# Kernel tuning notes

Hardware: AMD Instinct MI355X
Metric: run time of the kernel (lower is better)

The kernel has to match this reference:

```python
import jax, jax.numpy as jnp
import numpy as np

B, S, FEAT, H, DK, MAX_ITEMS = 8, 1024, 512, 8, 64, 200
LN_EPS = 1e-5
NEG = -999999999.0


def _build_mask(seq_len):
    # rows before T = S-(maxItems+1) cannot see the tail block [T:];
    # tail rows T..S-2 cannot see columns >= their own index (strict upper wedge).
    T = seq_len - (MAX_ITEMS + 1)
    i = jnp.arange(seq_len)[:, None]
    j = jnp.arange(seq_len)[None, :]
    blocked = ((i < T) & (j >= T)) | ((i >= T) & (i <= seq_len - 2) & (j >= i))
    return jnp.where(blocked, NEG, 0.0).astype(jnp.float32)  # [S, S]


def setup_inputs() -> dict:
    key = jax.random.key(0)
    ks = jax.random.split(key, 6)
    def init(k, shape, fan_in):
        return (jax.random.normal(k, shape, jnp.float32) / np.sqrt(fan_in)).astype(jnp.float32)
    return {
        "x": jax.random.normal(ks[0], (B, S, FEAT), jnp.float32),
        "ln_gamma": jnp.ones((FEAT,), jnp.float32),
        "ln_beta": jnp.zeros((FEAT,), jnp.float32),
        "WQ": init(ks[1], (H, FEAT, DK), FEAT), "bq": jnp.zeros((H, DK), jnp.float32),
        "WK": init(ks[2], (H, FEAT, DK), FEAT), "bk": jnp.zeros((H, DK), jnp.float32),
        "WV": init(ks[3], (H, FEAT, DK), FEAT), "bv": jnp.zeros((H, DK), jnp.float32),
        "WO": init(ks[4], (H * DK, FEAT), H * DK), "bO": jnp.zeros((FEAT,), jnp.float32),
    }


def reference(x, ln_gamma, ln_beta, WQ, bq, WK, bk, WV, bv, WO, bO):
    b, s, f = x.shape
    # Pre-LN
    mu = jnp.mean(x, axis=-1, keepdims=True)
    var = jnp.mean((x - mu) ** 2, axis=-1, keepdims=True)
    xn = (x - mu) / jnp.sqrt(var + LN_EPS) * ln_gamma + ln_beta
    # per-head projections, heads stacked: [B, H, S, DK]
    q = jnp.einsum('bsf,hfd->bhsd', xn, WQ) + bq[None, :, None, :]
    k = jnp.einsum('bsf,hfd->bhsd', xn, WK) + bk[None, :, None, :]
    v = jnp.einsum('bsf,hfd->bhsd', xn, WV) + bv[None, :, None, :]
    scores = jnp.einsum('bhsd,bhtd->bhst', q, k) / np.sqrt(DK).astype(np.float32)
    scores = scores + _build_mask(s)[None, None, :, :]
    attn = jax.nn.softmax(scores, axis=-1)
    z = jnp.einsum('bhst,bhtd->bhsd', attn, v)           # [B, H, S, DK]
    z = jnp.transpose(z, (0, 2, 1, 3)).reshape(b, s, -1)  # concat heads -> [B, S, H*DK]
    return z @ WO + bO
```

## Files before the change

### kernel.cpp

```cpp
#include <hip/hip_runtime.h>

#define S_LEN 1024
#define FEATN 512
#define NH    8
#define DKN   64
#define T_CUT 823
#define LDP   76

typedef __attribute__((ext_vector_type(8))) short v8s;
typedef __attribute__((ext_vector_type(4))) float v4f;
typedef unsigned short u16;

__device__ __forceinline__ float bf2f(u16 u) {
    unsigned v = ((unsigned)u) << 16; float f; __builtin_memcpy(&f, &v, 4); return f;
}
__device__ __forceinline__ u16 f2bf(float f) {
    unsigned v; __builtin_memcpy(&v, &f, 4);
    v += 0x7fffu + ((v >> 16) & 1u);
    return (u16)(v >> 16);
}
__device__ __forceinline__ v4f mfma16(v8s a, v8s b, v4f c) {
    return __builtin_amdgcn_mfma_f32_16x16x32_bf16(a, b, c, 0, 0, 0);
}
__device__ __forceinline__ unsigned cvt_pk_bf16(float a, float b) {
    unsigned r;
    asm("v_cvt_pk_bf16_f32 %0, %1, %2" : "=v"(r) : "v"(a), "v"(b));
    return r;
}

__device__ __forceinline__ int sniff_f32(const void* x) {
    const u16* xs = (const u16*)x;
    int wild = 0;
    #pragma unroll
    for (int i = 0; i < 64; i++) {
        float v = bf2f(xs[i]);
        float a = fabsf(v);
        wild |= (!(a <= 256.f)) | ((v != 0.f) & (a <= 1e-9f));
    }
    return wild;
}

__device__ __forceinline__ float read_in(const void* p, long idx, int fl) {
    return fl ? ((const float*)p)[idx] : bf2f(((const u16*)p)[idx]);
}

__global__ __launch_bounds__(256) void prep_kernel(
    const void* __restrict__ x, const void* __restrict__ lg,
    const void* __restrict__ lb,
    const void* __restrict__ WQ, const void* __restrict__ WK,
    const void* __restrict__ WV, const void* __restrict__ WO,
    u16* __restrict__ xn, u16* __restrict__ BtQKV, u16* __restrict__ BtO)
{
    __shared__ u16 ld[64 * 68];
    const int fl = sniff_f32(x);
    const int b = blockIdx.x, t = threadIdx.x;
    if (b < 192) {
        const int which = b >> 6, rem = b & 63, h = rem >> 3, ktile = rem & 7;
        const void* W = which == 0 ? WQ : (which == 1 ? WK : WV);
        const float sc = (which == 0) ? 0.125f : 1.f;
        #pragma unroll
        for (int i = 0; i < 16; i++) {
            int idx = i * 256 + t, r = idx >> 6, c = idx & 63;
            float v = read_in(W, (long)h * 512 * 64 + (long)(ktile * 64 + r) * 64 + c, fl);
            ld[c * 68 + r] = f2bf(v * sc);
        }
        __syncthreads();
        #pragma unroll
        for (int i = 0; i < 16; i++) {
            int idx = i * 256 + t, d = idx >> 6, kk = idx & 63;
            BtQKV[(long)(which * 512 + h * 64 + d) * 512 + ktile * 64 + kk] = ld[d * 68 + kk];
        }
    } else if (b < 256) {
        const int b2 = b - 192, ntile = b2 >> 3, ktile = b2 & 7;
        #pragma unroll
        for (int i = 0; i < 16; i++) {
            int idx = i * 256 + t, r = idx >> 6, c = idx & 63;
            float v = read_in(WO, (long)(ktile * 64 + r) * 512 + ntile * 64 + c, fl);
            ld[c * 68 + r] = f2bf(v);
        }
        __syncthreads();
        #pragma unroll
        for (int i = 0; i < 16; i++) {
            int idx = i * 256 + t, d = idx >> 6, kk = idx & 63;
            BtO[(long)(ntile * 64 + d) * 512 + ktile * 64 + kk] = ld[d * 68 + kk];
        }
    } else {
        const int w = t >> 6, l = t & 63;
        const int row = (b - 256) * 4 + w;
        float f[8];
        if (fl) {
            const float4* x4 = (const float4*)((const float*)x + (size_t)row * FEATN);
            float4 p0 = x4[l * 2], p1 = x4[l * 2 + 1];
            f[0] = p0.x; f[1] = p0.y; f[2] = p0.z; f[3] = p0.w;
            f[4] = p1.x; f[5] = p1.y; f[6] = p1.z; f[7] = p1.w;
        } else {
            const u16* xu = (const u16*)x + (size_t)row * FEATN + l * 8;
            #pragma unroll
            for (int j = 0; j < 8; j++) f[j] = bf2f(xu[j]);
        }
        float s = 0.f, sq = 0.f;
        #pragma unroll
        for (int j = 0; j < 8; j++) { s += f[j]; sq += f[j] * f[j]; }
        #pragma unroll
        for (int sh = 1; sh < 64; sh <<= 1) { s += __shfl_xor(s, sh); sq += __shfl_xor(sq, sh); }
        const float mu = s * (1.f / 512.f);
        const float var = sq * (1.f / 512.f) - mu * mu;
        const float rstd = rsqrtf(var + 1e-5f);
        u16 o8[8];
        #pragma unroll
        for (int j = 0; j < 8; j++) {
            float gg = read_in(lg, l * 8 + j, fl), bb = read_in(lb, l * 8 + j, fl);
            o8[j] = f2bf((f[j] - mu) * rstd * gg + bb);
        }
        *(v8s*)&xn[(size_t)row * FEATN + l * 8] = *(v8s*)o8;
    }
}

__global__ __launch_bounds__(256) void gemm128(
    const void* __restrict__ x,
    const u16* __restrict__ A, const u16* __restrict__ Bt,
    int N, int K, int mode,
    const void* __restrict__ bq, const void* __restrict__ bk,
    const void* __restrict__ bv,
    u16* __restrict__ qp, u16* __restrict__ kw, u16* __restrict__ vt,
    const void* __restrict__ bO, void* __restrict__ out)
{
    __shared__ __attribute__((aligned(16))) u16 lA[2][128 * 32];
    __shared__ __attribute__((aligned(16))) u16 lB[2][128 * 32];
    const int fl = sniff_f32(x);
    const int bid = blockIdx.x;
    const int xcd = bid & 7, sidx = bid >> 3;
    const int m0 = ((sidx & 7) + xcd * 8) * 128;
    const int n0 = (sidx >> 3) * 128;
    const int t = threadIdx.x;
    const int w = t >> 6, l = t & 63, quad = l >> 4, lr = l & 15;
    const int wr = w >> 1, wc = w & 1;
    v4f acc[4][4] = {};
    const int grow = w * 32 + (l >> 2);
    const int gcol = (l & 3) * 8;
    const u16* Ab = A  + (long)m0 * K;
    const u16* Bb = Bt + (long)n0 * K;

    auto stage = [&](int q, int k0) {
        #pragma unroll
        for (int i = 0; i < 2; i++) {
            __builtin_amdgcn_global_load_lds(
                (const __attribute__((address_space(1))) void*)
                    (Ab + (long)(grow + i * 16) * K + k0 + gcol),
                (__attribute__((address_space(3))) void*)&lA[q][(w * 32 + i * 16) * 32],
                16, 0, 0);
            __builtin_amdgcn_global_load_lds(
                (const __attribute__((address_space(1))) void*)
                    (Bb + (long)(grow + i * 16) * K + k0 + gcol),
                (__attribute__((address_space(3))) void*)&lB[q][(w * 32 + i * 16) * 32],
                16, 0, 0);
        }
    };
    stage(0, 0);
    __syncthreads();
    int cur = 0;
    for (int k0 = 0; k0 < K; k0 += 32) {
        if (k0 + 32 < K) stage(cur ^ 1, k0 + 32);
        v8s af[4], bf[4];
        #pragma unroll
        for (int i = 0; i < 4; i++) {
            af[i] = *(v8s*)&lA[cur][(wr * 64 + i * 16 + lr) * 32 + quad * 8];
            bf[i] = *(v8s*)&lB[cur][(wc * 64 + i * 16 + lr) * 32 + quad * 8];
        }
        #pragma unroll
        for (int i = 0; i < 4; i++)
            #pragma unroll
            for (int j = 0; j < 4; j++)
                acc[i][j] = mfma16(af[i], bf[j], acc[i][j]);
        __syncthreads();
        cur ^= 1;
    }
    #pragma unroll
    for (int i = 0; i < 4; i++)
    #pragma unroll
    for (int j = 0; j < 4; j++) {
        const int mbase = m0 + wr * 64 + i * 16 + quad * 4;
        const int n = n0 + wc * 64 + j * 16 + lr;
        if (mode == 0) {
            const int which = n >> 9, nn = n & 511, h = nn >> 6, d = nn & 63;
            const void* bias = which == 0 ? bq : (which == 1 ? bk : bv);
            const float bs = read_in(bias, nn, fl) * ((which == 0) ? 0.125f : 1.f);
            const int b = mbase >> 10, s = mbase & 1023;
            if (which != 1) {
                u16 v4_[4];
                #pragma unroll
                for (int r = 0; r < 4; r++) v4_[r] = f2bf(acc[i][j][r] + bs);
                u16* dstT = (which == 0) ? qp : vt;
                *(uint2*)&dstT[((size_t)((b * NH + h) * DKN + d)) * S_LEN + s] =
                    *(const uint2*)v4_;
            } else {
                #pragma unroll
                for (int r = 0; r < 4; r++)
                    kw[(((long)(b * NH + h)) * S_LEN + (s + r)) * DKN + d] =
                        f2bf(acc[i][j][r] + bs);
            }
        } else {
            const float bb = read_in(bO, n, fl);
            #pragma unroll
            for (int r = 0; r < 4; r++) {
                float ov = acc[i][j][r] + bb;
                if (fl) ((float*)out)[(long)(mbase + r) * N + n] = ov;
                else    ((u16*)out)[(long)(mbase + r) * N + n] = f2bf(ov);
            }
        }
    }
}

__global__ __launch_bounds__(256) void attn_kernel(
    const u16* __restrict__ qp, const u16* __restrict__ kw,
    const u16* __restrict__ vt, u16* __restrict__ zw)
{
    __shared__ __attribute__((aligned(16))) u16 lk[64 * LDP];
    __shared__ __attribute__((aligned(16))) u16 lv[64 * LDP];
    __shared__ __attribute__((aligned(16))) u16 lp[4][16 * LDP];
    const int bid = blockIdx.x;
    const int bh = bid & 63, qt = bid >> 6;
    const int q0 = qt * 64, qmax = q0 + 63;
    const int t = threadIdx.x, w = t >> 6, l = t & 63, quad = l >> 4, lr = l & 15;
    const int srow = t >> 2, scg = t & 3;
    const u16* Qp = qp + (size_t)bh * S_LEN * DKN;
    const u16* Kg = kw + (size_t)bh * S_LEN * DKN;
    const u16* Vt = vt + (size_t)bh * S_LEN * DKN;
    v8s aq[2];
    #pragma unroll
    for (int kf = 0; kf < 2; kf++) {
        u16 tmp[8];
        #pragma unroll
        for (int j = 0; j < 8; j++)
            tmp[j] = Qp[(size_t)(kf * 32 + quad * 8 + j) * S_LEN + q0 + w * 16 + lr];
        __builtin_memcpy(&aq[kf], tmp, 16);
    }
    v4f o[4] = {};
    v4f o1 = {};
    v8s vone;
    #pragma unroll
    for (int j = 0; j < 8; j++) vone[j] = (short)0x3f80;
    const int iq = q0 + w * 16 + quad * 4;
    const int i_row = q0 + w * 16 + lr;
    const int jlim = (i_row < T_CUT) ? T_CUT
                   : ((i_row <= S_LEN - 2) ? i_row : 0x40000000);
    const int mx_ = (T_CUT > qmax) ? T_CUT : qmax;
    const int ntiles = (qmax > S_LEN - 2) ? 16 : ((mx_ + 63) >> 6);
    v8s kr0 = *(const v8s*)&Kg[srow * DKN + scg * 8];
    v8s kr1 = *(const v8s*)&Kg[srow * DKN + 32 + scg * 8];
    v8s vr0 = *(const v8s*)&Vt[srow * S_LEN + scg * 8];
    v8s vr1 = *(const v8s*)&Vt[srow * S_LEN + 32 + scg * 8];

    for (int it = 0; it < ntiles; ++it) {
        const int kt0 = it * 64;
        __syncthreads();
        *(v8s*)&lk[srow * LDP + scg * 8]      = kr0;
        *(v8s*)&lk[srow * LDP + 32 + scg * 8] = kr1;
        *(v8s*)&lv[srow * LDP + scg * 8]      = vr0;
        *(v8s*)&lv[srow * LDP + 32 + scg * 8] = vr1;
        __syncthreads();
        if (it + 1 < ntiles) {
            kr0 = *(const v8s*)&Kg[(kt0 + 64 + srow) * DKN + scg * 8];
            kr1 = *(const v8s*)&Kg[(kt0 + 64 + srow) * DKN + 32 + scg * 8];
            vr0 = *(const v8s*)&Vt[srow * S_LEN + kt0 + 64 + scg * 8];
            vr1 = *(const v8s*)&Vt[srow * S_LEN + kt0 + 96 + scg * 8];
        }
        v4f sf[4];
        __builtin_amdgcn_s_setprio(1);
        #pragma unroll
        for (int cb = 0; cb < 4; cb++) {
            v8s b0 = *(v8s*)&lk[(cb * 16 + lr) * LDP + quad * 8];
            v8s b1 = *(v8s*)&lk[(cb * 16 + lr) * LDP + 32 + quad * 8];
            v4f z = {};
            z = mfma16(b0, aq[0], z);
            z = mfma16(b1, aq[1], z);
            sf[cb] = z;
        }
        __builtin_amdgcn_s_setprio(0);
        u16* lpw = lp[w];
        const int kt63 = kt0 + 63;
        const bool tmask = ((q0 < T_CUT) && (kt63 >= T_CUT)) ||
                           ((qmax >= T_CUT) && (kt63 >= q0));
        const int jbase = jlim - kt0 - quad * 4;
        #pragma unroll
        for (int cb = 0; cb < 4; cb++) {
            float e[4];
            #pragma unroll
            for (int r = 0; r < 4; r++) {
                float ev = __expf(sf[cb][r]);
                if (tmask) ev = (cb * 16 + r >= jbase) ? 0.f : ev;
                e[r] = ev;
            }
            uint2 pk;
            pk.x = cvt_pk_bf16(e[0], e[1]);
            pk.y = cvt_pk_bf16(e[2], e[3]);
            *(uint2*)&lpw[lr * LDP + cb * 16 + quad * 4] = pk;
        }
        __asm__ __volatile__("s_waitcnt lgkmcnt(0)" ::: "memory");
        __builtin_amdgcn_sched_barrier(0);
        __builtin_amdgcn_s_setprio(1);
        #pragma unroll
        for (int ks = 0; ks < 2; ks++) {
            v8s ap = *(v8s*)&lpw[lr * LDP + ks * 32 + quad * 8];
            #pragma unroll
            for (int db = 0; db < 4; db++) {
                v8s bv_ = *(v8s*)&lv[(db * 16 + lr) * LDP + ks * 32 + quad * 8];
                o[db] = mfma16(ap, bv_, o[db]);
            }
            o1 = mfma16(ap, vone, o1);
        }
        __builtin_amdgcn_s_setprio(0);
    }
    const int b = bh >> 3, h = bh & 7;
    #pragma unroll
    for (int r = 0; r < 4; r++) {
        const float inv = 1.f / o1[r];
        const int i = iq + r;
        #pragma unroll
        for (int db = 0; db < 4; db++)
            zw[((size_t)b * S_LEN + i) * (NH * DKN) + h * DKN + db * 16 + lr] =
                f2bf(o[db][r] * inv);
    }
}

extern "C" void kernel_launch(void* const* d_in, const int* in_sizes, int n_in,
                              void* d_out, int out_size, void* d_ws, size_t ws_size,
                              hipStream_t stream) {
    const void* x  = d_in[0];
    const void* lg = d_in[1];
    const void* lb = d_in[2];
    const void* WQ = d_in[3];
    const void* bq = d_in[4];
    const void* WK = d_in[5];
    const void* bk = d_in[6];
    const void* WV = d_in[7];
    const void* bv = d_in[8];
    const void* WO = d_in[9];
    const void* bO = d_in[10];

    char* p = (char*)d_ws;
    u16* xn      = (u16*)p;  p += (size_t)8192 * 512 * 2;
    u16* qp      = (u16*)p;  p += (size_t)4194304 * 2;
    u16* kw      = (u16*)p;  p += (size_t)4194304 * 2;
    u16* vt      = (u16*)p;  p += (size_t)4194304 * 2;
    u16* zw      = (u16*)p;  p += (size_t)8192 * 512 * 2;
    u16* BtQKV   = (u16*)p;  p += (size_t)1536 * 512 * 2;
    u16* BtO     = (u16*)p;  p += (size_t)512 * 512 * 2;

    prep_kernel<<<2304, 256, 0, stream>>>(x, lg, lb, WQ, WK, WV, WO, xn, BtQKV, BtO);
    gemm128<<<768, 256, 0, stream>>>(x, xn, BtQKV, 1536, 512, 0,
                                     bq, bk, bv, qp, kw, vt, nullptr, nullptr);
    attn_kernel<<<1024, 256, 0, stream>>>(qp, kw, vt, zw);
    gemm128<<<256, 256, 0, stream>>>(x, zw, BtO, 512, 512, 1,
                                     nullptr, nullptr, nullptr,
                                     nullptr, nullptr, nullptr, bO, d_out);
}
```

Before: 187.5 us.

## Keep softmax probabilities in registers by permuting V load layout to match MFMA fragments

Drops the per-wave LDS staging buffer for the exponentiated scores. The P fragments are packed directly from the QK^T MFMA accumulator registers into the A operand of the PV MFMA. To keep the contraction consistent, the global loads of V are reshuffled into four 4-element pieces so the LDS column order matches the register layout of P. This removes an LDS write, a wait and an LDS read per tile, but the V global loads become narrower (8-byte instead of 16-byte) and more numerous.

```diff
diff --git a/kernel.cpp b/kernel.cpp
--- a/kernel.cpp
+++ b/kernel.cpp
@@ -217,7 +217,6 @@
 {
     __shared__ __attribute__((aligned(16))) u16 lk[64 * LDP];
     __shared__ __attribute__((aligned(16))) u16 lv[64 * LDP];
-    __shared__ __attribute__((aligned(16))) u16 lp[4][16 * LDP];
     const int bid = blockIdx.x;
     const int bh = bid & 63, qt = bid >> 6;
     const int q0 = qt * 64, qmax = q0 + 63;
@@ -246,24 +245,37 @@
                    : ((i_row <= S_LEN - 2) ? i_row : 0x40000000);
     const int mx_ = (T_CUT > qmax) ? T_CUT : qmax;
     const int ntiles = (qmax > S_LEN - 2) ? 16 : ((mx_ + 63) >> 6);
+    const int vs = 4 * scg;
     v8s kr0 = *(const v8s*)&Kg[srow * DKN + scg * 8];
     v8s kr1 = *(const v8s*)&Kg[srow * DKN + 32 + scg * 8];
-    v8s vr0 = *(const v8s*)&Vt[srow * S_LEN + scg * 8];
-    v8s vr1 = *(const v8s*)&Vt[srow * S_LEN + 32 + scg * 8];
+    uint2 va0 = *(const uint2*)&Vt[srow * S_LEN + vs];
+    uint2 va1 = *(const uint2*)&Vt[srow * S_LEN + 16 + vs];
+    uint2 vb0 = *(const uint2*)&Vt[srow * S_LEN + 32 + vs];
+    uint2 vb1 = *(const uint2*)&Vt[srow * S_LEN + 48 + vs];
 
     for (int it = 0; it < ntiles; ++it) {
         const int kt0 = it * 64;
         __syncthreads();
         *(v8s*)&lk[srow * LDP + scg * 8]      = kr0;
         *(v8s*)&lk[srow * LDP + 32 + scg * 8] = kr1;
-        *(v8s*)&lv[srow * LDP + scg * 8]      = vr0;
-        *(v8s*)&lv[srow * LDP + 32 + scg * 8] = vr1;
+        {
+            unsigned wA[4] = {va0.x, va0.y, va1.x, va1.y};
+            unsigned wB[4] = {vb0.x, vb0.y, vb1.x, vb1.y};
+            v8s vrA, vrB;
+            __builtin_memcpy(&vrA, wA, 16);
+            __builtin_memcpy(&vrB, wB, 16);
+            *(v8s*)&lv[srow * LDP + scg * 8]      = vrA;
+            *(v8s*)&lv[srow * LDP + 32 + scg * 8] = vrB;
+        }
         __syncthreads();
         if (it + 1 < ntiles) {
             kr0 = *(const v8s*)&Kg[(kt0 + 64 + srow) * DKN + scg * 8];
             kr1 = *(const v8s*)&Kg[(kt0 + 64 + srow) * DKN + 32 + scg * 8];
-            vr0 = *(const v8s*)&Vt[srow * S_LEN + kt0 + 64 + scg * 8];
-            vr1 = *(const v8s*)&Vt[srow * S_LEN + kt0 + 96 + scg * 8];
+            const u16* vrow = &Vt[srow * S_LEN + kt0 + 64];
+            va0 = *(const uint2*)(vrow + vs);
+            va1 = *(const uint2*)(vrow + 16 + vs);
+            vb0 = *(const uint2*)(vrow + 32 + vs);
+            vb1 = *(const uint2*)(vrow + 48 + vs);
         }
         v4f sf[4];
         __builtin_amdgcn_s_setprio(1);
@@ -277,11 +289,11 @@
             sf[cb] = z;
         }
         __builtin_amdgcn_s_setprio(0);
-        u16* lpw = lp[w];
         const int kt63 = kt0 + 63;
         const bool tmask = ((q0 < T_CUT) && (kt63 >= T_CUT)) ||
                            ((qmax >= T_CUT) && (kt63 >= q0));
         const int jbase = jlim - kt0 - quad * 4;
+        unsigned pu[4][2];
         #pragma unroll
         for (int cb = 0; cb < 4; cb++) {
             float e[4];
@@ -291,24 +303,29 @@
                 if (tmask) ev = (cb * 16 + r >= jbase) ? 0.f : ev;
                 e[r] = ev;
             }
-            uint2 pk;
-            pk.x = cvt_pk_bf16(e[0], e[1]);
-            pk.y = cvt_pk_bf16(e[2], e[3]);
-            *(uint2*)&lpw[lr * LDP + cb * 16 + quad * 4] = pk;
-        }
-        __asm__ __volatile__("s_waitcnt lgkmcnt(0)" ::: "memory");
-        __builtin_amdgcn_sched_barrier(0);
+            pu[cb][0] = cvt_pk_bf16(e[0], e[1]);
+            pu[cb][1] = cvt_pk_bf16(e[2], e[3]);
+        }
+        v8s ap0, ap1;
+        {
+            unsigned a0_[4] = {pu[0][0], pu[0][1], pu[1][0], pu[1][1]};
+            unsigned a1_[4] = {pu[2][0], pu[2][1], pu[3][0], pu[3][1]};
+            __builtin_memcpy(&ap0, a0_, 16);
+            __builtin_memcpy(&ap1, a1_, 16);
+        }
         __builtin_amdgcn_s_setprio(1);
         #pragma unroll
-        for (int ks = 0; ks < 2; ks++) {
-            v8s ap = *(v8s*)&lpw[lr * LDP + ks * 32 + quad * 8];
-            #pragma unroll
-            for (int db = 0; db < 4; db++) {
-                v8s bv_ = *(v8s*)&lv[(db * 16 + lr) * LDP + ks * 32 + quad * 8];
-                o[db] = mfma16(ap, bv_, o[db]);
-            }
-            o1 = mfma16(ap, vone, o1);
-        }
+        for (int db = 0; db < 4; db++) {
+            v8s bv0 = *(v8s*)&lv[(db * 16 + lr) * LDP + quad * 8];
+            o[db] = mfma16(ap0, bv0, o[db]);
+        }
+        o1 = mfma16(ap0, vone, o1);
+        #pragma unroll
+        for (int db = 0; db < 4; db++) {
+            v8s bv1 = *(v8s*)&lv[(db * 16 + lr) * LDP + 32 + quad * 8];
+            o[db] = mfma16(ap1, bv1, o[db]);
+        }
+        o1 = mfma16(ap1, vone, o1);
         __builtin_amdgcn_s_setprio(0);
     }
     const int b = bh >> 3, h = bh & 7;
```

Result: faster. 176.0 us (-6.1%).
